# Kernel tuning notes

Hardware: AMD Instinct MI355X
Metric: run time of the kernel (lower is better)

Reference implementation:

```python
import jax, jax.numpy as jnp
import numpy as np

BN_EPS = 1e-5


def _batch_norm(h, gamma, beta):
    # training-mode BatchNorm1d over the node dimension (biased variance)
    mu = jnp.mean(h, axis=0)
    var = jnp.mean((h - mu) ** 2, axis=0)
    return (h - mu) * jax.lax.rsqrt(var + BN_EPS) * gamma + beta


def setup_inputs() -> dict:
    key = jax.random.key(0)
    ks = jax.random.split(key, 6)
    N, E, D, H = 50000, 800000, 128, 256
    x = jax.random.normal(ks[0], (N, D), dtype=jnp.float32)
    edge_index = jax.random.randint(ks[1], (2, E), 0, N, dtype=jnp.int64)
    batch = jnp.zeros((N,), dtype=jnp.int64)
    eps = jnp.zeros((1,), dtype=jnp.float32)  # train_eps=True, init 0
    W1 = jax.random.normal(ks[2], (D, H), dtype=jnp.float32) / np.sqrt(D)
    gamma1 = jnp.ones((H,), dtype=jnp.float32)
    beta1 = jnp.zeros((H,), dtype=jnp.float32)
    W2 = jax.random.normal(ks[3], (H, H), dtype=jnp.float32) / np.sqrt(H)
    gamma2 = jnp.ones((H,), dtype=jnp.float32)
    beta2 = jnp.zeros((H,), dtype=jnp.float32)
    return {"x": x, "edge_index": edge_index, "batch": batch, "eps": eps,
            "W1": W1, "gamma1": gamma1, "beta1": beta1,
            "W2": W2, "gamma2": gamma2, "beta2": beta2}


def reference(x, edge_index, batch, eps, W1, gamma1, beta1, W2, gamma2, beta2):
    N = x.shape[0]
    src, dst = edge_index[0], edge_index[1]
    # GIN aggregation: sum of neighbor features (scatter-add over dst)
    agg = jax.ops.segment_sum(x[src], dst, num_segments=N)  # [N, D]
    h = (1.0 + eps[0]) * x + agg
    # MLP: Linear -> BN -> ReLU -> Linear -> BN
    h = jax.nn.relu(_batch_norm(h @ W1, gamma1, beta1))
    h = _batch_norm(h @ W2, gamma2, beta2)
    # outer non-linearity in GIN_layer.forward
    return jax.nn.relu(h)
```

## Files before the change

### kernel.cpp

```cpp
#include <hip/hip_runtime.h>

#define N_NODES 50000
#define D_IN    128
#define D_H     256
#define MT      64
#define NGB     782
#define NPART   NGB

#define NBKT    391
#define BKT_CAP 3072
#define EPB     2048

typedef short s16x8 __attribute__((ext_vector_type(8)));
typedef short s16x4 __attribute__((ext_vector_type(4)));
typedef float f32x4 __attribute__((ext_vector_type(4)));

__device__ inline ushort f2bf(float f) {
    uint u = __float_as_uint(f);
    return (ushort)((u + 0x7FFFu + ((u >> 16) & 1u)) >> 16);
}
__device__ inline float bf2f(ushort u) { return __uint_as_float(((uint)u) << 16); }

__global__ __launch_bounds__(256) void prep_kernel(const float* __restrict__ x,
                                                   const float* __restrict__ W1,
                                                   const float* __restrict__ W2,
                                                   ushort* __restrict__ xB,
                                                   ushort* __restrict__ Wp1,
                                                   ushort* __restrict__ Wp2,
                                                   int* __restrict__ bucket_fill) {
    int bid = blockIdx.x, tid = threadIdx.x;
    if (bid < 3125) {
        int i = bid * 256 + tid;
        float4 a = ((const float4*)x)[(size_t)i * 2];
        float4 b = ((const float4*)x)[(size_t)i * 2 + 1];
        s16x8 o;
        o[0] = (short)f2bf(a.x); o[1] = (short)f2bf(a.y);
        o[2] = (short)f2bf(a.z); o[3] = (short)f2bf(a.w);
        o[4] = (short)f2bf(b.x); o[5] = (short)f2bf(b.y);
        o[6] = (short)f2bf(b.z); o[7] = (short)f2bf(b.w);
        ((s16x8*)xB)[i] = o;
    } else if (bid < 3173) {
        int t = (bid - 3125) * 256 + tid;
        const float* W; ushort* Wp; int u;
        if (t < 4096) { W = W1; Wp = Wp1; u = t; }
        else          { W = W2; Wp = Wp2; u = t - 4096; }
        int l = u & 63, gs = u >> 6;
        int g = gs & 15, s = gs >> 4;
        int col = g * 16 + (l & 15), q = l >> 4;
        s16x8 o;
#pragma unroll
        for (int j = 0; j < 8; j++) {
            int k = s * 32 + q * 8 + j;
            o[j] = (short)f2bf(W[(size_t)k * D_H + col]);
        }
        *(s16x8*)(Wp + (size_t)u * 8) = o;
    } else {
        for (int i = tid; i < NBKT; i += 256) bucket_fill[i] = 0;
    }
}

__global__ __launch_bounds__(256) void bucket_kernel(const int* __restrict__ ei,
                                                     int* __restrict__ bucket_fill,
                                                     uint* __restrict__ bucket_buf, int E) {
    __shared__ int cnt[NBKT], gbase[NBKT], fill2[NBKT];
    int tid = threadIdx.x;
    int e0 = blockIdx.x * EPB;
    for (int i = tid; i < NBKT; i += 256) { cnt[i] = 0; fill2[i] = 0; }
    __syncthreads();
    int dstv[8];
#pragma unroll
    for (int j = 0; j < 8; j++) {
        int e = e0 + j * 256 + tid;
        dstv[j] = (e < E) ? ei[E + e] : -1;
        if (dstv[j] >= 0) atomicAdd(&cnt[dstv[j] >> 7], 1);
    }
    __syncthreads();
    for (int i = tid; i < NBKT; i += 256) {
        int c = cnt[i];
        gbase[i] = c ? atomicAdd(&bucket_fill[i], c) : 0;
    }
    __syncthreads();
#pragma unroll
    for (int j = 0; j < 8; j++) {
        int e = e0 + j * 256 + tid;
        if (dstv[j] >= 0) {
            int src = ei[e];
            int b = dstv[j] >> 7;
            int p = atomicAdd(&fill2[b], 1);
            bucket_buf[(size_t)b * BKT_CAP + gbase[b] + p] =
                ((uint)(dstv[j] & 127) << 16) | (uint)src;
        }
    }
}

__global__ __launch_bounds__(512) void gather_bucket_kernel(const ushort* __restrict__ xB,
                                                            const float* __restrict__ eps,
                                                            const int* __restrict__ bucket_fill,
                                                            const uint* __restrict__ bucket_buf,
                                                            ushort* __restrict__ h) {
    __shared__ uint   raw[BKT_CAP];
    __shared__ ushort srt[BKT_CAP];
    __shared__ int cnt[128], off[128], f2[128];
    int b = blockIdx.x, tid = threadIdx.x;
    int n = bucket_fill[b];
    if (n > BKT_CAP) n = BKT_CAP;
    for (int i = tid; i < n; i += 512) raw[i] = bucket_buf[(size_t)b * BKT_CAP + i];
    if (tid < 128) { cnt[tid] = 0; f2[tid] = 0; }
    __syncthreads();
    for (int i = tid; i < n; i += 512) atomicAdd(&cnt[raw[i] >> 16], 1);
    __syncthreads();
    if (tid < 128) off[tid] = cnt[tid];
    __syncthreads();
    for (int s2 = 1; s2 < 128; s2 <<= 1) {
        int t = (tid < 128 && tid >= s2) ? off[tid - s2] : 0;
        __syncthreads();
        if (tid < 128) off[tid] += t;
        __syncthreads();
    }
    for (int i = tid; i < n; i += 512) {
        uint r = raw[i];
        int d = r >> 16;
        int p = atomicAdd(&f2[d], 1);
        srt[(off[d] - cnt[d]) + p] = (ushort)(r & 0xFFFFu);
    }
    __syncthreads();

    int grp = tid >> 5, lane = tid & 31;
    int c = lane << 2;
    float s = 1.0f + eps[0];
    for (int dl = grp; dl < 128; dl += 16) {
        int d = b * 128 + dl;
        if (d >= N_NODES) break;
        int st = off[dl] - cnt[dl], cn = cnt[dl];
        s16x4 sv = *(const s16x4*)(xB + (size_t)d * D_IN + c);
        float a0 = bf2f((ushort)sv[0]) * s, a1 = bf2f((ushort)sv[1]) * s,
              a2 = bf2f((ushort)sv[2]) * s, a3 = bf2f((ushort)sv[3]) * s;
        int j = 0;
        for (; j + 3 < cn; j += 4) {
            int s0 = srt[st + j],     s1 = srt[st + j + 1];
            int s2 = srt[st + j + 2], s3 = srt[st + j + 3];
            s16x4 v0 = *(const s16x4*)(xB + (size_t)s0 * D_IN + c);
            s16x4 v1 = *(const s16x4*)(xB + (size_t)s1 * D_IN + c);
            s16x4 v2 = *(const s16x4*)(xB + (size_t)s2 * D_IN + c);
            s16x4 v3 = *(const s16x4*)(xB + (size_t)s3 * D_IN + c);
            a0 += bf2f((ushort)v0[0]) + bf2f((ushort)v1[0]) + bf2f((ushort)v2[0]) + bf2f((ushort)v3[0]);
            a1 += bf2f((ushort)v0[1]) + bf2f((ushort)v1[1]) + bf2f((ushort)v2[1]) + bf2f((ushort)v3[1]);
            a2 += bf2f((ushort)v0[2]) + bf2f((ushort)v1[2]) + bf2f((ushort)v2[2]) + bf2f((ushort)v3[2]);
            a3 += bf2f((ushort)v0[3]) + bf2f((ushort)v1[3]) + bf2f((ushort)v2[3]) + bf2f((ushort)v3[3]);
        }
        for (; j < cn; j++) {
            int s0 = srt[st + j];
            s16x4 v0 = *(const s16x4*)(xB + (size_t)s0 * D_IN + c);
            a0 += bf2f((ushort)v0[0]); a1 += bf2f((ushort)v0[1]);
            a2 += bf2f((ushort)v0[2]); a3 += bf2f((ushort)v0[3]);
        }
        s16x4 o;
        o[0] = (short)f2bf(a0); o[1] = (short)f2bf(a1);
        o[2] = (short)f2bf(a2); o[3] = (short)f2bf(a3);
        *(s16x4*)(h + (size_t)d * D_IN + c) = o;
    }
}

__global__ __launch_bounds__(512) void gemm1_kernel(const ushort* __restrict__ hB,
                                                    const ushort* __restrict__ Wp,
                                                    ushort* __restrict__ h1B,
                                                    float* __restrict__ partial) {
    __shared__ ushort A[MT * D_IN];
    int tid = threadIdx.x, lane = tid & 63, w = tid >> 6;
    int row0 = blockIdx.x * MT;
    int m = lane & 15, q = lane >> 4;
    const s16x8* B = (const s16x8*)Wp;
    s16x8 bf[8];
#pragma unroll
    for (int s = 0; s < 4; s++)
#pragma unroll
        for (int f = 0; f < 2; f++)
            bf[s * 2 + f] = B[(s * 16 + w * 2 + f) * 64 + lane];
    for (int i = tid; i < 1024; i += 512) {
        int r = i >> 4, cb = (i & 15) << 4;
        int row = row0 + r;
        s16x8 v = {};
        if (row < N_NODES) v = *(const s16x8*)(hB + (size_t)row * D_IN + (cb >> 1));
        *(s16x8*)((char*)A + r * 256 + (cb ^ ((r & 7) << 4))) = v;
    }
    __syncthreads();
    int sw = (m & 7) << 4;
    f32x4 acc[4][2] = {};
#pragma unroll
    for (int s = 0; s < 4; s++) {
        int co = (s * 64 + q * 16) ^ sw;
        s16x8 a0 = *(const s16x8*)((char*)A + (m     ) * 256 + co);
        s16x8 a1 = *(const s16x8*)((char*)A + (m + 16) * 256 + co);
        s16x8 a2 = *(const s16x8*)((char*)A + (m + 32) * 256 + co);
        s16x8 a3 = *(const s16x8*)((char*)A + (m + 48) * 256 + co);
#pragma unroll
        for (int f = 0; f < 2; f++) {
            acc[0][f] = __builtin_amdgcn_mfma_f32_16x16x32_bf16(a0, bf[s * 2 + f], acc[0][f], 0, 0, 0);
            acc[1][f] = __builtin_amdgcn_mfma_f32_16x16x32_bf16(a1, bf[s * 2 + f], acc[1][f], 0, 0, 0);
            acc[2][f] = __builtin_amdgcn_mfma_f32_16x16x32_bf16(a2, bf[s * 2 + f], acc[2][f], 0, 0, 0);
            acc[3][f] = __builtin_amdgcn_mfma_f32_16x16x32_bf16(a3, bf[s * 2 + f], acc[3][f], 0, 0, 0);
        }
    }
#pragma unroll
    for (int f = 0; f < 2; f++) {
        int col = (w * 2 + f) * 16 + m;
        float s1 = 0.f, s2 = 0.f;
#pragma unroll
        for (int t = 0; t < 4; t++) {
#pragma unroll
            for (int j = 0; j < 4; j++) {
                float v = acc[t][f][j];
                int row = row0 + t * 16 + q * 4 + j;
                if (row < N_NODES) h1B[(size_t)row * D_H + col] = f2bf(v);
                s1 += v; s2 = fmaf(v, v, s2);
            }
        }
        s1 += __shfl_xor(s1, 16, 64); s1 += __shfl_xor(s1, 32, 64);
        s2 += __shfl_xor(s2, 16, 64); s2 += __shfl_xor(s2, 32, 64);
        if (lane < 16) {
            partial[(size_t)blockIdx.x * 512 + col] = s1;
            partial[(size_t)blockIdx.x * 512 + 256 + col] = s2;
        }
    }
}

__global__ __launch_bounds__(256) void bn_finalize_kernel(const float* __restrict__ partial,
                                                          const float* __restrict__ gamma,
                                                          const float* __restrict__ beta,
                                                          float* __restrict__ scale,
                                                          float* __restrict__ shift) {
    int s = blockIdx.x;
    int tid = threadIdx.x;
    float sum = 0.f, sq = 0.f;
    for (int b = tid; b < NPART; b += 256) {
        sum += partial[(size_t)b * 512 + s];
        sq  += partial[(size_t)b * 512 + 256 + s];
    }
    __shared__ float rs[256], rq[256];
    rs[tid] = sum; rq[tid] = sq;
    __syncthreads();
    for (int off = 128; off > 0; off >>= 1) {
        if (tid < off) { rs[tid] += rs[tid + off]; rq[tid] += rq[tid + off]; }
        __syncthreads();
    }
    if (tid == 0) {
        float inv  = 1.0f / (float)N_NODES;
        float mean = rs[0] * inv;
        float var  = rq[0] * inv - mean * mean;
        float sc   = gamma[s] * rsqrtf(var + 1e-5f);
        scale[s] = sc;
        shift[s] = fmaf(-mean, sc, beta[s]);
    }
}

__global__ __launch_bounds__(512) void gemm2_kernel(const ushort* __restrict__ h1B,
                                                    const ushort* __restrict__ Wp,
                                                    const float* __restrict__ scale1,
                                                    const float* __restrict__ shift1,
                                                    ushort* __restrict__ h2B,
                                                    float* __restrict__ partial) {
    __shared__ ushort A[MT * D_H];
    int tid = threadIdx.x, lane = tid & 63, w = tid >> 6;
    int row0 = blockIdx.x * MT;
    int m = lane & 15, q = lane >> 4;
    const s16x8* B = (const s16x8*)Wp;
    s16x8 bf[16];
#pragma unroll
    for (int s = 0; s < 8; s++)
#pragma unroll
        for (int f = 0; f < 2; f++)
            bf[s * 2 + f] = B[(s * 16 + w * 2 + f) * 64 + lane];
    for (int i = tid; i < 2048; i += 512) {
        int r = i >> 5, cb = (i & 31) << 4;
        int row = row0 + r, c0 = cb >> 1;
        s16x8 o = {};
        if (row < N_NODES) {
            s16x8 in = *(const s16x8*)(h1B + (size_t)row * D_H + c0);
            float4 sc0 = *(const float4*)(scale1 + c0), sc1 = *(const float4*)(scale1 + c0 + 4);
            float4 sh0 = *(const float4*)(shift1 + c0), sh1 = *(const float4*)(shift1 + c0 + 4);
            o[0] = (short)f2bf(fmaxf(fmaf(bf2f((ushort)in[0]), sc0.x, sh0.x), 0.f));
            o[1] = (short)f2bf(fmaxf(fmaf(bf2f((ushort)in[1]), sc0.y, sh0.y), 0.f));
            o[2] = (short)f2bf(fmaxf(fmaf(bf2f((ushort)in[2]), sc0.z, sh0.z), 0.f));
            o[3] = (short)f2bf(fmaxf(fmaf(bf2f((ushort)in[3]), sc0.w, sh0.w), 0.f));
            o[4] = (short)f2bf(fmaxf(fmaf(bf2f((ushort)in[4]), sc1.x, sh1.x), 0.f));
            o[5] = (short)f2bf(fmaxf(fmaf(bf2f((ushort)in[5]), sc1.y, sh1.y), 0.f));
            o[6] = (short)f2bf(fmaxf(fmaf(bf2f((ushort)in[6]), sc1.z, sh1.z), 0.f));
            o[7] = (short)f2bf(fmaxf(fmaf(bf2f((ushort)in[7]), sc1.w, sh1.w), 0.f));
        }
        *(s16x8*)((char*)A + r * 512 + (cb ^ ((r & 7) << 4))) = o;
    }
    __syncthreads();
    int sw = (m & 7) << 4;
    f32x4 acc[4][2] = {};
#pragma unroll
    for (int s = 0; s < 8; s++) {
        int co = (s * 64 + q * 16) ^ sw;
        s16x8 a0 = *(const s16x8*)((char*)A + (m     ) * 512 + co);
        s16x8 a1 = *(const s16x8*)((char*)A + (m + 16) * 512 + co);
        s16x8 a2 = *(const s16x8*)((char*)A + (m + 32) * 512 + co);
        s16x8 a3 = *(const s16x8*)((char*)A + (m + 48) * 512 + co);
#pragma unroll
        for (int f = 0; f < 2; f++) {
            acc[0][f] = __builtin_amdgcn_mfma_f32_16x16x32_bf16(a0, bf[s * 2 + f], acc[0][f], 0, 0, 0);
            acc[1][f] = __builtin_amdgcn_mfma_f32_16x16x32_bf16(a1, bf[s * 2 + f], acc[1][f], 0, 0, 0);
            acc[2][f] = __builtin_amdgcn_mfma_f32_16x16x32_bf16(a2, bf[s * 2 + f], acc[2][f], 0, 0, 0);
            acc[3][f] = __builtin_amdgcn_mfma_f32_16x16x32_bf16(a3, bf[s * 2 + f], acc[3][f], 0, 0, 0);
        }
    }
#pragma unroll
    for (int f = 0; f < 2; f++) {
        int col = (w * 2 + f) * 16 + m;
        float s1 = 0.f, s2 = 0.f;
#pragma unroll
        for (int t = 0; t < 4; t++) {
#pragma unroll
            for (int j = 0; j < 4; j++) {
                float v = acc[t][f][j];
                int row = row0 + t * 16 + q * 4 + j;
                if (row < N_NODES) h2B[(size_t)row * D_H + col] = f2bf(v);
                s1 += v; s2 = fmaf(v, v, s2);
            }
        }
        s1 += __shfl_xor(s1, 16, 64); s1 += __shfl_xor(s1, 32, 64);
        s2 += __shfl_xor(s2, 16, 64); s2 += __shfl_xor(s2, 32, 64);
        if (lane < 16) {
            partial[(size_t)blockIdx.x * 512 + col] = s1;
            partial[(size_t)blockIdx.x * 512 + 256 + col] = s2;
        }
    }
}

__global__ __launch_bounds__(256) void bn2_apply_kernel(const ushort* __restrict__ h2B,
                                                        const float* __restrict__ scale,
                                                        const float* __restrict__ shift,
                                                        float* __restrict__ out, int total8) {
    int i = blockIdx.x * 256 + threadIdx.x;
    if (i >= total8) return;
    s16x8 v = ((const s16x8*)h2B)[i];
    int c = (i & 31) << 3;
    float4 sc0 = *(const float4*)(scale + c), sc1 = *(const float4*)(scale + c + 4);
    float4 sh0 = *(const float4*)(shift + c), sh1 = *(const float4*)(shift + c + 4);
    float4 o0, o1;
    o0.x = fmaxf(fmaf(bf2f((ushort)v[0]), sc0.x, sh0.x), 0.f);
    o0.y = fmaxf(fmaf(bf2f((ushort)v[1]), sc0.y, sh0.y), 0.f);
    o0.z = fmaxf(fmaf(bf2f((ushort)v[2]), sc0.z, sh0.z), 0.f);
    o0.w = fmaxf(fmaf(bf2f((ushort)v[3]), sc0.w, sh0.w), 0.f);
    o1.x = fmaxf(fmaf(bf2f((ushort)v[4]), sc1.x, sh1.x), 0.f);
    o1.y = fmaxf(fmaf(bf2f((ushort)v[5]), sc1.y, sh1.y), 0.f);
    o1.z = fmaxf(fmaf(bf2f((ushort)v[6]), sc1.z, sh1.z), 0.f);
    o1.w = fmaxf(fmaf(bf2f((ushort)v[7]), sc1.w, sh1.w), 0.f);
    ((float4*)out)[(size_t)i * 2]     = o0;
    ((float4*)out)[(size_t)i * 2 + 1] = o1;
}

extern "C" void kernel_launch(void* const* d_in, const int* in_sizes, int n_in,
                              void* d_out, int out_size, void* d_ws, size_t ws_size,
                              hipStream_t stream) {
    const float* x      = (const float*)d_in[0];
    const int*   ei     = (const int*)d_in[1];
    const float* eps    = (const float*)d_in[3];
    const float* W1     = (const float*)d_in[4];
    const float* gamma1 = (const float*)d_in[5];
    const float* beta1  = (const float*)d_in[6];
    const float* W2     = (const float*)d_in[7];
    const float* gamma2 = (const float*)d_in[8];
    const float* beta2  = (const float*)d_in[9];
    int E = in_sizes[1] / 2;

    char* ws = (char*)d_ws;
    ushort* xB     = (ushort*)(ws);
    float*  partial= (float*)(ws);
    ushort* hB     = (ushort*)(ws + 12800000);
    ushort* h1B    = (ushort*)(ws + 25600000);
    ushort* h2B    = (ushort*)(ws + 51200000);
    float*  stats  = (float*)(ws + 76800000);
    ushort* Wp1    = (ushort*)(ws + 76804096);
    ushort* Wp2    = (ushort*)(ws + 76869632);
    float* scale1 = stats, *shift1 = stats + 256, *scale2 = stats + 512, *shift2 = stats + 768;
    float* out = (float*)d_out;

    int*  bucket_fill = (int*)(ws + 51200000);
    uint* bucket_buf  = (uint*)(ws + 51202048);

    prep_kernel<<<3174, 256, 0, stream>>>(x, W1, W2, xB, Wp1, Wp2, bucket_fill);
    bucket_kernel<<<(E + EPB - 1) / EPB, 256, 0, stream>>>(ei, bucket_fill, bucket_buf, E);
    gather_bucket_kernel<<<NBKT, 512, 0, stream>>>(xB, eps, bucket_fill, bucket_buf, hB);

    gemm1_kernel<<<NGB, 512, 0, stream>>>(hB, Wp1, h1B, partial);
    bn_finalize_kernel<<<D_H, 256, 0, stream>>>(partial, gamma1, beta1, scale1, shift1);
    gemm2_kernel<<<NGB, 512, 0, stream>>>(h1B, Wp2, scale1, shift1, h2B, partial);
    bn_finalize_kernel<<<D_H, 256, 0, stream>>>(partial, gamma2, beta2, scale2, shift2);
    bn2_apply_kernel<<<(1600000 + 255) / 256, 256, 0, stream>>>(h2B, scale2, shift2, out, 1600000);
}
```

Measured before the change: 121.8 us.

## Fuse neighbor gather into first GEMM via shared-memory tile

Merges the bucket gather kernel with the first GEMM. Each block aggregates its 128 destination rows straight into a swizzled LDS tile and then runs MFMA on 128 rows, instead of writing hB to global memory and reloading it. This removes one kernel launch and the global round trip of the aggregated features. In exchange the block uses more LDS (32KB extra), which lowers occupancy, and there are only 391 blocks, so the GEMM work is spread over fewer, larger blocks. The partial-stats buffer is moved to its own region, and bn_finalize now takes the partition count as a parameter.

Result: slower. 134.9 us (+10.8%).

```diff
diff --git a/kernel.cpp b/kernel.cpp
--- a/kernel.cpp
+++ b/kernel.cpp
@@ -5,8 +5,6 @@
 #define D_H     256
 #define MT      64
 #define NGB     782
-#define NPART   NGB
-
 #define NBKT    391
 #define BKT_CAP 3072
 #define EPB     2048
@@ -93,15 +91,28 @@
     }
 }
 
-__global__ __launch_bounds__(512) void gather_bucket_kernel(const ushort* __restrict__ xB,
-                                                            const float* __restrict__ eps,
-                                                            const int* __restrict__ bucket_fill,
-                                                            const uint* __restrict__ bucket_buf,
-                                                            ushort* __restrict__ h) {
+__global__ __launch_bounds__(512) void gather_gemm1_kernel(const ushort* __restrict__ xB,
+                                                           const float* __restrict__ eps,
+                                                           const int* __restrict__ bucket_fill,
+                                                           const uint* __restrict__ bucket_buf,
+                                                           const ushort* __restrict__ Wp,
+                                                           ushort* __restrict__ h1B,
+                                                           float* __restrict__ partial) {
     __shared__ uint   raw[BKT_CAP];
     __shared__ ushort srt[BKT_CAP];
     __shared__ int cnt[128], off[128], f2[128];
+    __shared__ ushort A[128 * D_IN];
     int b = blockIdx.x, tid = threadIdx.x;
+    int lane = tid & 63, w = tid >> 6;
+    int m = lane & 15, q = lane >> 4;
+    const s16x8* B = (const s16x8*)Wp;
+    s16x8 bf[8];
+#pragma unroll
+    for (int s = 0; s < 4; s++)
+#pragma unroll
+        for (int f = 0; f < 2; f++)
+            bf[s * 2 + f] = B[(s * 16 + w * 2 + f) * 64 + lane];
+
     int n = bucket_fill[b];
     if (n > BKT_CAP) n = BKT_CAP;
     for (int i = tid; i < n; i += 512) raw[i] = bucket_buf[(size_t)b * BKT_CAP + i];
@@ -125,88 +136,65 @@
     }
     __syncthreads();
 
-    int grp = tid >> 5, lane = tid & 31;
-    int c = lane << 2;
-    float s = 1.0f + eps[0];
-    for (int dl = grp; dl < 128; dl += 16) {
-        int d = b * 128 + dl;
-        if (d >= N_NODES) break;
-        int st = off[dl] - cnt[dl], cn = cnt[dl];
-        s16x4 sv = *(const s16x4*)(xB + (size_t)d * D_IN + c);
-        float a0 = bf2f((ushort)sv[0]) * s, a1 = bf2f((ushort)sv[1]) * s,
-              a2 = bf2f((ushort)sv[2]) * s, a3 = bf2f((ushort)sv[3]) * s;
-        int j = 0;
-        for (; j + 3 < cn; j += 4) {
-            int s0 = srt[st + j],     s1 = srt[st + j + 1];
-            int s2 = srt[st + j + 2], s3 = srt[st + j + 3];
-            s16x4 v0 = *(const s16x4*)(xB + (size_t)s0 * D_IN + c);
-            s16x4 v1 = *(const s16x4*)(xB + (size_t)s1 * D_IN + c);
-            s16x4 v2 = *(const s16x4*)(xB + (size_t)s2 * D_IN + c);
-            s16x4 v3 = *(const s16x4*)(xB + (size_t)s3 * D_IN + c);
-            a0 += bf2f((ushort)v0[0]) + bf2f((ushort)v1[0]) + bf2f((ushort)v2[0]) + bf2f((ushort)v3[0]);
-            a1 += bf2f((ushort)v0[1]) + bf2f((ushort)v1[1]) + bf2f((ushort)v2[1]) + bf2f((ushort)v3[1]);
-            a2 += bf2f((ushort)v0[2]) + bf2f((ushort)v1[2]) + bf2f((ushort)v2[2]) + bf2f((ushort)v3[2]);
-            a3 += bf2f((ushort)v0[3]) + bf2f((ushort)v1[3]) + bf2f((ushort)v2[3]) + bf2f((ushort)v3[3]);
-        }
-        for (; j < cn; j++) {
-            int s0 = srt[st + j];
-            s16x4 v0 = *(const s16x4*)(xB + (size_t)s0 * D_IN + c);
-            a0 += bf2f((ushort)v0[0]); a1 += bf2f((ushort)v0[1]);
-            a2 += bf2f((ushort)v0[2]); a3 += bf2f((ushort)v0[3]);
-        }
-        s16x4 o;
-        o[0] = (short)f2bf(a0); o[1] = (short)f2bf(a1);
-        o[2] = (short)f2bf(a2); o[3] = (short)f2bf(a3);
-        *(s16x4*)(h + (size_t)d * D_IN + c) = o;
-    }
-}
-
-__global__ __launch_bounds__(512) void gemm1_kernel(const ushort* __restrict__ hB,
-                                                    const ushort* __restrict__ Wp,
-                                                    ushort* __restrict__ h1B,
-                                                    float* __restrict__ partial) {
-    __shared__ ushort A[MT * D_IN];
-    int tid = threadIdx.x, lane = tid & 63, w = tid >> 6;
-    int row0 = blockIdx.x * MT;
-    int m = lane & 15, q = lane >> 4;
-    const s16x8* B = (const s16x8*)Wp;
-    s16x8 bf[8];
-#pragma unroll
-    for (int s = 0; s < 4; s++)
-#pragma unroll
-        for (int f = 0; f < 2; f++)
-            bf[s * 2 + f] = B[(s * 16 + w * 2 + f) * 64 + lane];
-    for (int i = tid; i < 1024; i += 512) {
-        int r = i >> 4, cb = (i & 15) << 4;
-        int row = row0 + r;
-        s16x8 v = {};
-        if (row < N_NODES) v = *(const s16x8*)(hB + (size_t)row * D_IN + (cb >> 1));
-        *(s16x8*)((char*)A + r * 256 + (cb ^ ((r & 7) << 4))) = v;
-    }
-    __syncthreads();
+    {
+        int grp = tid >> 5, lane32 = tid & 31;
+        int c = lane32 << 2;
+        float s = 1.0f + eps[0];
+        for (int dl = grp; dl < 128; dl += 16) {
+            int d = b * 128 + dl;
+            s16x4 o = {};
+            if (d < N_NODES) {
+                int st = off[dl] - cnt[dl], cn = cnt[dl];
+                s16x4 sv = *(const s16x4*)(xB + (size_t)d * D_IN + c);
+                float a0 = bf2f((ushort)sv[0]) * s, a1 = bf2f((ushort)sv[1]) * s,
+                      a2 = bf2f((ushort)sv[2]) * s, a3 = bf2f((ushort)sv[3]) * s;
+                int j = 0;
+                for (; j + 3 < cn; j += 4) {
+                    int s0 = srt[st + j],     s1 = srt[st + j + 1];
+                    int s2 = srt[st + j + 2], s3 = srt[st + j + 3];
+                    s16x4 v0 = *(const s16x4*)(xB + (size_t)s0 * D_IN + c);
+                    s16x4 v1 = *(const s16x4*)(xB + (size_t)s1 * D_IN + c);
+                    s16x4 v2 = *(const s16x4*)(xB + (size_t)s2 * D_IN + c);
+                    s16x4 v3 = *(const s16x4*)(xB + (size_t)s3 * D_IN + c);
+                    a0 += bf2f((ushort)v0[0]) + bf2f((ushort)v1[0]) + bf2f((ushort)v2[0]) + bf2f((ushort)v3[0]);
+                    a1 += bf2f((ushort)v0[1]) + bf2f((ushort)v1[1]) + bf2f((ushort)v2[1]) + bf2f((ushort)v3[1]);
+                    a2 += bf2f((ushort)v0[2]) + bf2f((ushort)v1[2]) + bf2f((ushort)v2[2]) + bf2f((ushort)v3[2]);
+                    a3 += bf2f((ushort)v0[3]) + bf2f((ushort)v1[3]) + bf2f((ushort)v2[3]) + bf2f((ushort)v3[3]);
+                }
+                for (; j < cn; j++) {
+                    int s0 = srt[st + j];
+                    s16x4 v0 = *(const s16x4*)(xB + (size_t)s0 * D_IN + c);
+                    a0 += bf2f((ushort)v0[0]); a1 += bf2f((ushort)v0[1]);
+                    a2 += bf2f((ushort)v0[2]); a3 += bf2f((ushort)v0[3]);
+                }
+                o[0] = (short)f2bf(a0); o[1] = (short)f2bf(a1);
+                o[2] = (short)f2bf(a2); o[3] = (short)f2bf(a3);
+            }
+            *(s16x4*)((char*)A + dl * 256 + ((c * 2) ^ ((dl & 7) << 4))) = o;
+        }
+    }
+    __syncthreads();
+
     int sw = (m & 7) << 4;
-    f32x4 acc[4][2] = {};
+    f32x4 acc[8][2] = {};
 #pragma unroll
     for (int s = 0; s < 4; s++) {
         int co = (s * 64 + q * 16) ^ sw;
-        s16x8 a0 = *(const s16x8*)((char*)A + (m     ) * 256 + co);
-        s16x8 a1 = *(const s16x8*)((char*)A + (m + 16) * 256 + co);
-        s16x8 a2 = *(const s16x8*)((char*)A + (m + 32) * 256 + co);
-        s16x8 a3 = *(const s16x8*)((char*)A + (m + 48) * 256 + co);
-#pragma unroll
-        for (int f = 0; f < 2; f++) {
-            acc[0][f] = __builtin_amdgcn_mfma_f32_16x16x32_bf16(a0, bf[s * 2 + f], acc[0][f], 0, 0, 0);
-            acc[1][f] = __builtin_amdgcn_mfma_f32_16x16x32_bf16(a1, bf[s * 2 + f], acc[1][f], 0, 0, 0);
-            acc[2][f] = __builtin_amdgcn_mfma_f32_16x16x32_bf16(a2, bf[s * 2 + f], acc[2][f], 0, 0, 0);
-            acc[3][f] = __builtin_amdgcn_mfma_f32_16x16x32_bf16(a3, bf[s * 2 + f], acc[3][f], 0, 0, 0);
-        }
-    }
+#pragma unroll
+        for (int t = 0; t < 8; t++) {
+            s16x8 a = *(const s16x8*)((char*)A + (m + t * 16) * 256 + co);
+#pragma unroll
+            for (int f = 0; f < 2; f++)
+                acc[t][f] = __builtin_amdgcn_mfma_f32_16x16x32_bf16(a, bf[s * 2 + f], acc[t][f], 0, 0, 0);
+        }
+    }
+    int row0 = b * 128;
 #pragma unroll
     for (int f = 0; f < 2; f++) {
         int col = (w * 2 + f) * 16 + m;
         float s1 = 0.f, s2 = 0.f;
 #pragma unroll
-        for (int t = 0; t < 4; t++) {
+        for (int t = 0; t < 8; t++) {
 #pragma unroll
             for (int j = 0; j < 4; j++) {
                 float v = acc[t][f][j];
@@ -218,13 +206,14 @@
         s1 += __shfl_xor(s1, 16, 64); s1 += __shfl_xor(s1, 32, 64);
         s2 += __shfl_xor(s2, 16, 64); s2 += __shfl_xor(s2, 32, 64);
         if (lane < 16) {
-            partial[(size_t)blockIdx.x * 512 + col] = s1;
-            partial[(size_t)blockIdx.x * 512 + 256 + col] = s2;
+            partial[(size_t)b * 512 + col] = s1;
+            partial[(size_t)b * 512 + 256 + col] = s2;
         }
     }
 }
 
 __global__ __launch_bounds__(256) void bn_finalize_kernel(const float* __restrict__ partial,
+                                                          int npart,
                                                           const float* __restrict__ gamma,
                                                           const float* __restrict__ beta,
                                                           float* __restrict__ scale,
@@ -232,7 +221,7 @@
     int s = blockIdx.x;
     int tid = threadIdx.x;
     float sum = 0.f, sq = 0.f;
-    for (int b = tid; b < NPART; b += 256) {
+    for (int b = tid; b < npart; b += 256) {
         sum += partial[(size_t)b * 512 + s];
         sq  += partial[(size_t)b * 512 + 256 + s];
     }
@@ -369,13 +358,12 @@
 
     char* ws = (char*)d_ws;
     ushort* xB     = (ushort*)(ws);
-    float*  partial= (float*)(ws);
-    ushort* hB     = (ushort*)(ws + 12800000);
     ushort* h1B    = (ushort*)(ws + 25600000);
     ushort* h2B    = (ushort*)(ws + 51200000);
     float*  stats  = (float*)(ws + 76800000);
     ushort* Wp1    = (ushort*)(ws + 76804096);
     ushort* Wp2    = (ushort*)(ws + 76869632);
+    float*  partial= (float*)(ws + 77001728);
     float* scale1 = stats, *shift1 = stats + 256, *scale2 = stats + 512, *shift2 = stats + 768;
     float* out = (float*)d_out;
 
@@ -384,11 +372,9 @@
 
     prep_kernel<<<3174, 256, 0, stream>>>(x, W1, W2, xB, Wp1, Wp2, bucket_fill);
     bucket_kernel<<<(E + EPB - 1) / EPB, 256, 0, stream>>>(ei, bucket_fill, bucket_buf, E);
-    gather_bucket_kernel<<<NBKT, 512, 0, stream>>>(xB, eps, bucket_fill, bucket_buf, hB);
-
-    gemm1_kernel<<<NGB, 512, 0, stream>>>(hB, Wp1, h1B, partial);
-    bn_finalize_kernel<<<D_H, 256, 0, stream>>>(partial, gamma1, beta1, scale1, shift1);
+    gather_gemm1_kernel<<<NBKT, 512, 0, stream>>>(xB, eps, bucket_fill, bucket_buf, Wp1, h1B, partial);
+    bn_finalize_kernel<<<D_H, 256, 0, stream>>>(partial, NBKT, gamma1, beta1, scale1, shift1);
     gemm2_kernel<<<NGB, 512, 0, stream>>>(h1B, Wp2, scale1, shift1, h2B, partial);
-    bn_finalize_kernel<<<D_H, 256, 0, stream>>>(partial, gamma2, beta2, scale2, shift2);
+    bn_finalize_kernel<<<D_H, 256, 0, stream>>>(partial, NGB, gamma2, beta2, scale2, shift2);
     bn2_apply_kernel<<<(1600000 + 255) / 256, 256, 0, stream>>>(h2B, scale2, shift2, out, 1600000);
 }
```

## Process two row tiles per gemm2 block with register prefetch of next tile

Applied to the files above, without the earlier changes.

gemm2 now handles 128 rows per block as two 64-row tiles, launching half as many blocks. The W2 fragments loaded into registers are reused across both tiles. The second tile's h1 rows are prefetched into registers while the first tile's MFMAs run, so global load latency overlaps compute. The trade-off is fewer blocks for occupancy and an extra barrier per block; partial-stat indexing is kept compatible with the finalize kernel.

Result: no change. 122.5 us (+0.6%).

```diff
diff --git a/kernel.cpp b/kernel.cpp
--- a/kernel.cpp
+++ b/kernel.cpp
@@ -5,8 +5,7 @@
 #define D_H     256
 #define MT      64
 #define NGB     782
-#define NPART   NGB
-
+#define NG2     391
 #define NBKT    391
 #define BKT_CAP 3072
 #define EPB     2048
@@ -225,6 +224,7 @@
 }
 
 __global__ __launch_bounds__(256) void bn_finalize_kernel(const float* __restrict__ partial,
+                                                          int npart,
                                                           const float* __restrict__ gamma,
                                                           const float* __restrict__ beta,
                                                           float* __restrict__ scale,
@@ -232,7 +232,7 @@
     int s = blockIdx.x;
     int tid = threadIdx.x;
     float sum = 0.f, sq = 0.f;
-    for (int b = tid; b < NPART; b += 256) {
+    for (int b = tid; b < npart; b += 256) {
         sum += partial[(size_t)b * 512 + s];
         sq  += partial[(size_t)b * 512 + 256 + s];
     }
@@ -259,10 +259,10 @@
                                                     const float* __restrict__ shift1,
                                                     ushort* __restrict__ h2B,
                                                     float* __restrict__ partial) {
-    __shared__ ushort A[MT * D_H];
+    __shared__ ushort A[64 * D_H];
     int tid = threadIdx.x, lane = tid & 63, w = tid >> 6;
-    int row0 = blockIdx.x * MT;
     int m = lane & 15, q = lane >> 4;
+    int r0 = tid >> 5, cb = (tid & 31) << 4, c0 = cb >> 1;
     const s16x8* B = (const s16x8*)Wp;
     s16x8 bf[16];
 #pragma unroll
@@ -270,27 +270,48 @@
 #pragma unroll
         for (int f = 0; f < 2; f++)
             bf[s * 2 + f] = B[(s * 16 + w * 2 + f) * 64 + lane];
-    for (int i = tid; i < 2048; i += 512) {
-        int r = i >> 5, cb = (i & 31) << 4;
-        int row = row0 + r, c0 = cb >> 1;
+
+    float4 sca = *(const float4*)(scale1 + c0), scb = *(const float4*)(scale1 + c0 + 4);
+    float4 sha = *(const float4*)(shift1 + c0), shb = *(const float4*)(shift1 + c0 + 4);
+
+    int base0 = blockIdx.x * 128;
+    int base1 = base0 + 64;
+    int sw = (m & 7) << 4;
+    s16x8 rg[4];
+
+#pragma unroll
+    for (int k = 0; k < 4; k++) {
+        int row = base0 + r0 + k * 16;
+        s16x8 v = {};
+        if (row < N_NODES) v = *(const s16x8*)(h1B + (size_t)row * D_H + c0);
+        rg[k] = v;
+    }
+#pragma unroll
+    for (int k = 0; k < 4; k++) {
+        int r = r0 + k * 16;
         s16x8 o = {};
-        if (row < N_NODES) {
-            s16x8 in = *(const s16x8*)(h1B + (size_t)row * D_H + c0);
-            float4 sc0 = *(const float4*)(scale1 + c0), sc1 = *(const float4*)(scale1 + c0 + 4);
-            float4 sh0 = *(const float4*)(shift1 + c0), sh1 = *(const float4*)(shift1 + c0 + 4);
-            o[0] = (short)f2bf(fmaxf(fmaf(bf2f((ushort)in[0]), sc0.x, sh0.x), 0.f));
-            o[1] = (short)f2bf(fmaxf(fmaf(bf2f((ushort)in[1]), sc0.y, sh0.y), 0.f));
-            o[2] = (short)f2bf(fmaxf(fmaf(bf2f((ushort)in[2]), sc0.z, sh0.z), 0.f));
-            o[3] = (short)f2bf(fmaxf(fmaf(bf2f((ushort)in[3]), sc0.w, sh0.w), 0.f));
-            o[4] = (short)f2bf(fmaxf(fmaf(bf2f((ushort)in[4]), sc1.x, sh1.x), 0.f));
-            o[5] = (short)f2bf(fmaxf(fmaf(bf2f((ushort)in[5]), sc1.y, sh1.y), 0.f));
-            o[6] = (short)f2bf(fmaxf(fmaf(bf2f((ushort)in[6]), sc1.z, sh1.z), 0.f));
-            o[7] = (short)f2bf(fmaxf(fmaf(bf2f((ushort)in[7]), sc1.w, sh1.w), 0.f));
+        if (base0 + r < N_NODES) {
+            o[0] = (short)f2bf(fmaxf(fmaf(bf2f((ushort)rg[k][0]), sca.x, sha.x), 0.f));
+            o[1] = (short)f2bf(fmaxf(fmaf(bf2f((ushort)rg[k][1]), sca.y, sha.y), 0.f));
+            o[2] = (short)f2bf(fmaxf(fmaf(bf2f((ushort)rg[k][2]), sca.z, sha.z), 0.f));
+            o[3] = (short)f2bf(fmaxf(fmaf(bf2f((ushort)rg[k][3]), sca.w, sha.w), 0.f));
+            o[4] = (short)f2bf(fmaxf(fmaf(bf2f((ushort)rg[k][4]), scb.x, shb.x), 0.f));
+            o[5] = (short)f2bf(fmaxf(fmaf(bf2f((ushort)rg[k][5]), scb.y, shb.y), 0.f));
+            o[6] = (short)f2bf(fmaxf(fmaf(bf2f((ushort)rg[k][6]), scb.z, shb.z), 0.f));
+            o[7] = (short)f2bf(fmaxf(fmaf(bf2f((ushort)rg[k][7]), scb.w, shb.w), 0.f));
         }
         *(s16x8*)((char*)A + r * 512 + (cb ^ ((r & 7) << 4))) = o;
     }
     __syncthreads();
-    int sw = (m & 7) << 4;
+
+#pragma unroll
+    for (int k = 0; k < 4; k++) {
+        int row = base1 + r0 + k * 16;
+        s16x8 v = {};
+        if (row < N_NODES) v = *(const s16x8*)(h1B + (size_t)row * D_H + c0);
+        rg[k] = v;
+    }
+
     f32x4 acc[4][2] = {};
 #pragma unroll
     for (int s = 0; s < 8; s++) {
@@ -307,6 +328,8 @@
             acc[3][f] = __builtin_amdgcn_mfma_f32_16x16x32_bf16(a3, bf[s * 2 + f], acc[3][f], 0, 0, 0);
         }
     }
+    __syncthreads();
+
 #pragma unroll
     for (int f = 0; f < 2; f++) {
         int col = (w * 2 + f) * 16 + m;
@@ -316,7 +339,7 @@
 #pragma unroll
             for (int j = 0; j < 4; j++) {
                 float v = acc[t][f][j];
-                int row = row0 + t * 16 + q * 4 + j;
+                int row = base0 + t * 16 + q * 4 + j;
                 if (row < N_NODES) h2B[(size_t)row * D_H + col] = f2bf(v);
                 s1 += v; s2 = fmaf(v, v, s2);
             }
@@ -324,8 +347,69 @@
         s1 += __shfl_xor(s1, 16, 64); s1 += __shfl_xor(s1, 32, 64);
         s2 += __shfl_xor(s2, 16, 64); s2 += __shfl_xor(s2, 32, 64);
         if (lane < 16) {
-            partial[(size_t)blockIdx.x * 512 + col] = s1;
-            partial[(size_t)blockIdx.x * 512 + 256 + col] = s2;
+            partial[((size_t)blockIdx.x * 2 + 0) * 512 + col] = s1;
+            partial[((size_t)blockIdx.x * 2 + 0) * 512 + 256 + col] = s2;
+        }
+    }
+
+#pragma unroll
+    for (int k = 0; k < 4; k++) {
+        int r = r0 + k * 16;
+        s16x8 o = {};
+        if (base1 + r < N_NODES) {
+            o[0] = (short)f2bf(fmaxf(fmaf(bf2f((ushort)rg[k][0]), sca.x, sha.x), 0.f));
+            o[1] = (short)f2bf(fmaxf(fmaf(bf2f((ushort)rg[k][1]), sca.y, sha.y), 0.f));
+            o[2] = (short)f2bf(fmaxf(fmaf(bf2f((ushort)rg[k][2]), sca.z, sha.z), 0.f));
+            o[3] = (short)f2bf(fmaxf(fmaf(bf2f((ushort)rg[k][3]), sca.w, sha.w), 0.f));
+            o[4] = (short)f2bf(fmaxf(fmaf(bf2f((ushort)rg[k][4]), scb.x, shb.x), 0.f));
+            o[5] = (short)f2bf(fmaxf(fmaf(bf2f((ushort)rg[k][5]), scb.y, shb.y), 0.f));
+            o[6] = (short)f2bf(fmaxf(fmaf(bf2f((ushort)rg[k][6]), scb.z, shb.z), 0.f));
+            o[7] = (short)f2bf(fmaxf(fmaf(bf2f((ushort)rg[k][7]), scb.w, shb.w), 0.f));
+        }
+        *(s16x8*)((char*)A + r * 512 + (cb ^ ((r & 7) << 4))) = o;
+    }
+    __syncthreads();
+
+#pragma unroll
+    for (int t = 0; t < 4; t++)
+#pragma unroll
+        for (int f = 0; f < 2; f++)
+            acc[t][f] = (f32x4){};
+#pragma unroll
+    for (int s = 0; s < 8; s++) {
+        int co = (s * 64 + q * 16) ^ sw;
+        s16x8 a0 = *(const s16x8*)((char*)A + (m     ) * 512 + co);
+        s16x8 a1 = *(const s16x8*)((char*)A + (m + 16) * 512 + co);
+        s16x8 a2 = *(const s16x8*)((char*)A + (m + 32) * 512 + co);
+        s16x8 a3 = *(const s16x8*)((char*)A + (m + 48) * 512 + co);
+#pragma unroll
+        for (int f = 0; f < 2; f++) {
+            acc[0][f] = __builtin_amdgcn_mfma_f32_16x16x32_bf16(a0, bf[s * 2 + f], acc[0][f], 0, 0, 0);
+            acc[1][f] = __builtin_amdgcn_mfma_f32_16x16x32_bf16(a1, bf[s * 2 + f], acc[1][f], 0, 0, 0);
+            acc[2][f] = __builtin_amdgcn_mfma_f32_16x16x32_bf16(a2, bf[s * 2 + f], acc[2][f], 0, 0, 0);
+            acc[3][f] = __builtin_amdgcn_mfma_f32_16x16x32_bf16(a3, bf[s * 2 + f], acc[3][f], 0, 0, 0);
+        }
+    }
+
+#pragma unroll
+    for (int f = 0; f < 2; f++) {
+        int col = (w * 2 + f) * 16 + m;
+        float s1 = 0.f, s2 = 0.f;
+#pragma unroll
+        for (int t = 0; t < 4; t++) {
+#pragma unroll
+            for (int j = 0; j < 4; j++) {
+                float v = acc[t][f][j];
+                int row = base1 + t * 16 + q * 4 + j;
+                if (row < N_NODES) h2B[(size_t)row * D_H + col] = f2bf(v);
+                s1 += v; s2 = fmaf(v, v, s2);
+            }
+        }
+        s1 += __shfl_xor(s1, 16, 64); s1 += __shfl_xor(s1, 32, 64);
+        s2 += __shfl_xor(s2, 16, 64); s2 += __shfl_xor(s2, 32, 64);
+        if (lane < 16) {
+            partial[((size_t)blockIdx.x * 2 + 1) * 512 + col] = s1;
+            partial[((size_t)blockIdx.x * 2 + 1) * 512 + 256 + col] = s2;
         }
     }
 }
@@ -387,8 +471,8 @@
     gather_bucket_kernel<<<NBKT, 512, 0, stream>>>(xB, eps, bucket_fill, bucket_buf, hB);
 
     gemm1_kernel<<<NGB, 512, 0, stream>>>(hB, Wp1, h1B, partial);
-    bn_finalize_kernel<<<D_H, 256, 0, stream>>>(partial, gamma1, beta1, scale1, shift1);
-    gemm2_kernel<<<NGB, 512, 0, stream>>>(h1B, Wp2, scale1, shift1, h2B, partial);
-    bn_finalize_kernel<<<D_H, 256, 0, stream>>>(partial, gamma2, beta2, scale2, shift2);
+    bn_finalize_kernel<<<D_H, 256, 0, stream>>>(partial, NGB, gamma1, beta1, scale1, shift1);
+    gemm2_kernel<<<NG2, 512, 0, stream>>>(h1B, Wp2, scale1, shift1, h2B, partial);
+    bn_finalize_kernel<<<D_H, 256, 0, stream>>>(partial, NGB, gamma2, beta2, scale2, shift2);
     bn2_apply_kernel<<<(1600000 + 255) / 256, 256, 0, stream>>>(h2B, scale2, shift2, out, 1600000);
 }
```
